# Optimization experiments

Measured on AMD Instinct MI355X. Metric: run time of the kernel, lower is better.

## Reference

```python
import jax, jax.numpy as jnp
import numpy as np

D_MODEL = 1024
NUM_HEADS = 16
HEAD_DIM = D_MODEL // NUM_HEADS


def setup_inputs() -> dict:
    key = jax.random.key(0)
    ks = jax.random.split(key, 9)
    B, S = 4, 2048
    scale = 1.0 / np.sqrt(D_MODEL)
    x = jax.random.normal(ks[0], (B, S, D_MODEL), dtype=jnp.float32)
    Wq = jax.random.normal(ks[1], (D_MODEL, D_MODEL), dtype=jnp.float32) * scale
    bq = jnp.zeros((D_MODEL,), dtype=jnp.float32)
    Wk = jax.random.normal(ks[2], (D_MODEL, D_MODEL), dtype=jnp.float32) * scale
    bk = jnp.zeros((D_MODEL,), dtype=jnp.float32)
    Wv = jax.random.normal(ks[3], (D_MODEL, D_MODEL), dtype=jnp.float32) * scale
    bv = jnp.zeros((D_MODEL,), dtype=jnp.float32)
    Wo = jax.random.normal(ks[4], (D_MODEL, D_MODEL), dtype=jnp.float32) * scale
    bo = jnp.zeros((D_MODEL,), dtype=jnp.float32)
    return {"x": x, "Wq": Wq, "bq": bq, "Wk": Wk, "bk": bk,
            "Wv": Wv, "bv": bv, "Wo": Wo, "bo": bo}


def reference(x, Wq, bq, Wk, bk, Wv, bv, Wo, bo):
    B, S, D = x.shape
    H, Hd = NUM_HEADS, HEAD_DIM
    # linear projections then split heads: [B,S,D] -> [B,H,S,Hd]
    def split(t):
        return t.reshape(B, S, H, Hd).transpose(0, 2, 1, 3)
    q = split(x @ Wq + bq)
    k = split(x @ Wk + bk)
    v = split(x @ Wv + bv)
    scores = jnp.einsum('bhsd,bhtd->bhst', q, k) / jnp.sqrt(
        jnp.asarray(Hd, dtype=jnp.float32))
    attn = jax.nn.softmax(scores, axis=-1)
    out = jnp.einsum('bhst,bhtd->bhsd', attn, v)  # [B,H,S,Hd]
    out = out.transpose(0, 2, 1, 3).reshape(B, S, D)
    return out @ Wo + bo
```

## Files before the change

kernel.cpp:

```cpp
#include <hip/hip_runtime.h>

#define DM 1024
#define NH 16
#define HD 64
#define SEQ 2048
#define BATCH 4
#define MROWS (BATCH*SEQ)

typedef short short8 __attribute__((ext_vector_type(8)));
typedef float f32x4 __attribute__((ext_vector_type(4)));
typedef unsigned short u16x8 __attribute__((ext_vector_type(8)));
typedef unsigned short u16x4 __attribute__((ext_vector_type(4)));

__device__ inline unsigned short f2b(float f) {
    union { float f; unsigned u; } v; v.f = f;
    unsigned r = v.u + 0x7fffu + ((v.u >> 16) & 1u);
    return (unsigned short)(r >> 16);
}

__device__ inline void gload_lds16(const void* g, void* l) {
    __builtin_amdgcn_global_load_lds(
        (const __attribute__((address_space(1))) void*)g,
        (__attribute__((address_space(3))) void*)l, 16, 0, 0);
}

__device__ inline unsigned cvt_pk_bf16(float lo, float hi) {
    unsigned r;
    asm("v_cvt_pk_bf16_f32 %0, %1, %2" : "=v"(r) : "v"(lo), "v"(hi));
    return r;
}

__global__ void k_cvt_x(const float* __restrict__ x, unsigned short* __restrict__ xb) {
    long i = ((long)blockIdx.x * 256 + threadIdx.x) * 8;
    float4 a = *reinterpret_cast<const float4*>(x + i);
    float4 b = *reinterpret_cast<const float4*>(x + i + 4);
    u16x8 o;
    o[0]=f2b(a.x); o[1]=f2b(a.y); o[2]=f2b(a.z); o[3]=f2b(a.w);
    o[4]=f2b(b.x); o[5]=f2b(b.y); o[6]=f2b(b.z); o[7]=f2b(b.w);
    *reinterpret_cast<u16x8*>(xb + i) = o;
}

__global__ void k_cvt_wT(const float* W0, const float* W1, const float* W2, const float* W3,
                         unsigned short* __restrict__ out) {
    const float* Ws[4] = {W0, W1, W2, W3};
    const float* W = Ws[blockIdx.z];
    unsigned short* o = out + (size_t)blockIdx.z * DM * DM;
    __shared__ float t[64][65];
    int tx = threadIdx.x & 15, ty = threadIdx.x >> 4;
    int nb = blockIdx.x * 64, kb = blockIdx.y * 64;
#pragma unroll
    for (int i = 0; i < 4; ++i) {
        int r = ty + 16 * i;
        float4 v = *reinterpret_cast<const float4*>(W + (size_t)(kb + r) * DM + nb + tx * 4);
        t[r][tx*4+0] = v.x; t[r][tx*4+1] = v.y; t[r][tx*4+2] = v.z; t[r][tx*4+3] = v.w;
    }
    __syncthreads();
#pragma unroll
    for (int i = 0; i < 4; ++i) {
        int r = ty + 16 * i;
        u16x4 pv;
#pragma unroll
        for (int j = 0; j < 4; ++j) pv[j] = f2b(t[tx*4+j][r]);
        *reinterpret_cast<u16x4*>(o + (size_t)(nb + r) * DM + kb + tx * 4) = pv;
    }
}

#define BM 128
#define BN 128
#define BK 64
#define QSCALE 0.1803368801f

__global__ __launch_bounds__(256) void k_gemm(const unsigned short* __restrict__ A,
                                              const unsigned short* __restrict__ Bt,
                                              const float* __restrict__ bias,
                                              unsigned short* __restrict__ outb,
                                              float* __restrict__ outf, int mode) {
    __shared__ unsigned short lds[BM*BK + BN*BK];
    unsigned short* lA = lds;
    unsigned short* lB = lds + BM*BK;
    int tid = threadIdx.x, lane = tid & 63, wv = tid >> 6;
    int wr = wv >> 1, wc = wv & 1;
    int c = lane & 15, g = lane >> 4;
    int m0 = blockIdx.x * BM, n0 = blockIdx.y * BN;
    f32x4 acc[4][4] = {};

    for (int kt = 0; kt < DM / BK; ++kt) {
#pragma unroll
        for (int it = 0; it < 4; ++it) {
            int sgi = it * 256 + tid;
            int row = sgi >> 3, blk = sgi & 7;
            int srcoff = kt * BK + ((blk ^ (row & 7)) << 3);
            gload_lds16(A  + (size_t)(m0 + row) * DM + srcoff, &lA[(it*256 + wv*64) * 8]);
            gload_lds16(Bt + (size_t)(n0 + row) * DM + srcoff, &lB[(it*256 + wv*64) * 8]);
        }
        __syncthreads();
#pragma unroll
        for (int ks = 0; ks < 2; ++ks) {
            short8 af[4], bf[4];
#pragma unroll
            for (int mi = 0; mi < 4; ++mi) {
                int row = wr*64 + mi*16 + c;
                af[mi] = *reinterpret_cast<const short8*>(&lA[row*64 + (((ks*4 + g) ^ (row & 7)) << 3)]);
            }
#pragma unroll
            for (int ni = 0; ni < 4; ++ni) {
                int row = wc*64 + ni*16 + c;
                bf[ni] = *reinterpret_cast<const short8*>(&lB[row*64 + (((ks*4 + g) ^ (row & 7)) << 3)]);
            }
#pragma unroll
            for (int mi = 0; mi < 4; ++mi)
#pragma unroll
                for (int ni = 0; ni < 4; ++ni)
                    acc[mi][ni] = __builtin_amdgcn_mfma_f32_16x16x32_bf16(af[mi], bf[ni], acc[mi][ni], 0, 0, 0);
        }
        __syncthreads();
    }

    if (mode == 2) {
        unsigned short* t = lds;
#pragma unroll
        for (int mi = 0; mi < 4; ++mi)
#pragma unroll
            for (int ni = 0; ni < 4; ++ni)
#pragma unroll
                for (int r = 0; r < 4; ++r) {
                    int lr = wr*64 + mi*16 + 4*g + r;
                    int lc = wc*64 + ni*16 + c;
                    t[lc*128 + lr] = f2b(acc[mi][ni][r] + bias[n0 + lc]);
                }
        __syncthreads();
#pragma unroll
        for (int i = 0; i < 8; ++i) {
            int idx = (i*256 + tid) * 8;
            int lc = idx >> 7, lr = idx & 127;
            int gcol = n0 + lc, grow = m0 + lr;
            int b = grow >> 11, s = grow & 2047, h = gcol >> 6, d = gcol & 63;
            *reinterpret_cast<u16x8*>(&outb[((size_t)((b*NH + h) << 6) + d) * SEQ + s]) =
                *reinterpret_cast<u16x8*>(&t[idx]);
        }
    }
}

__global__ __launch_bounds__(512, 2) void k_gemm256(const unsigned short* __restrict__ A,
                                                    const unsigned short* __restrict__ Bt,
                                                    const float* __restrict__ b0,
                                                    const float* __restrict__ b1,
                                                    unsigned short* __restrict__ oQ,
                                                    unsigned short* __restrict__ oK,
                                                    float* __restrict__ oF,
                                                    int perXcd, int mode) {
    __shared__ unsigned short L[2][2][2][128*64];
    int tid = threadIdx.x, lane = tid & 63, wid = tid >> 6;
    int wm = wid >> 2, wn = wid & 3;
    int c = lane & 15, g = lane >> 4;

    int bid = blockIdx.x;
    int swz = (bid & 7) * perXcd + (bid >> 3);
    int mb = swz & 31, nb = swz >> 5;
    int m0 = mb * 256, n0 = nb * 256;

    int idx0 = tid, idx1 = 512 + tid;
    int r0 = idx0 >> 3, k0 = idx0 & 7;
    int r1 = idx1 >> 3, k1 = idx1 & 7;

    auto stageHalf = [&](int buf, int ab, int half, int kt) {
        const unsigned short* src = ab ? Bt : A;
        int base = (ab ? n0 : m0) + half * 128;
        gload_lds16(src + (size_t)(base + r0) * DM + kt*64 + ((k0 ^ (r0 & 7)) << 3),
                    &L[buf][ab][half][idx0 * 8]);
        gload_lds16(src + (size_t)(base + r1) * DM + kt*64 + ((k1 ^ (r1 & 7)) << 3),
                    &L[buf][ab][half][idx1 * 8]);
    };

    f32x4 acc[8][4] = {};
    short8 af[4][2], bf0[2][2], bf1[2][2];

    stageHalf(0, 0, 0, 0); stageHalf(0, 1, 0, 0);
    stageHalf(0, 0, 1, 0); stageHalf(0, 1, 1, 0);

#define RDA(BUF, I, MH, KS) (*reinterpret_cast<const short8*>(                         \
        &L[BUF][0][wm][((MH)*64 + (I)*16 + c)*64 +                                     \
                       ((((KS)*4 + g) ^ (((MH)*64 + (I)*16 + c) & 7)) << 3)]))
#define RDB(BUF, J, NHh, KS) (*reinterpret_cast<const short8*>(                        \
        &L[BUF][1][wn>>1][((wn&1)*64 + (NHh)*32 + (J)*16 + c)*64 +                     \
                       ((((KS)*4 + g) ^ (((wn&1)*64 + (NHh)*32 + (J)*16 + c) & 7)) << 3)]))

    for (int it = 0; it < 16; ++it) {
        int cur = it & 1, nxt = cur ^ 1;

        if (it < 15) {
            stageHalf(nxt, 0, 0, it+1); stageHalf(nxt, 1, 0, it+1);
            stageHalf(nxt, 0, 1, it+1); stageHalf(nxt, 1, 1, it+1);
            asm volatile("s_waitcnt vmcnt(8)" ::: "memory");
        } else {
            asm volatile("s_waitcnt vmcnt(0)" ::: "memory");
        }
        __builtin_amdgcn_s_barrier();

#pragma unroll
        for (int i = 0; i < 4; ++i) { af[i][0] = RDA(cur, i, 0, 0); af[i][1] = RDA(cur, i, 0, 1); }
#pragma unroll
        for (int j = 0; j < 2; ++j) { bf0[j][0] = RDB(cur, j, 0, 0); bf0[j][1] = RDB(cur, j, 0, 1); }
        __builtin_amdgcn_s_setprio(1);
#pragma unroll
        for (int i = 0; i < 4; ++i)
#pragma unroll
            for (int j = 0; j < 2; ++j) {
                acc[i][j] = __builtin_amdgcn_mfma_f32_16x16x32_bf16(af[i][0], bf0[j][0], acc[i][j], 0, 0, 0);
                acc[i][j] = __builtin_amdgcn_mfma_f32_16x16x32_bf16(af[i][1], bf0[j][1], acc[i][j], 0, 0, 0);
            }
        __builtin_amdgcn_s_setprio(0);

#pragma unroll
        for (int i = 0; i < 4; ++i) { af[i][0] = RDA(cur, i, 1, 0); af[i][1] = RDA(cur, i, 1, 1); }
        __builtin_amdgcn_s_setprio(1);
#pragma unroll
        for (int i = 0; i < 4; ++i)
#pragma unroll
            for (int j = 0; j < 2; ++j) {
                acc[4+i][j] = __builtin_amdgcn_mfma_f32_16x16x32_bf16(af[i][0], bf0[j][0], acc[4+i][j], 0, 0, 0);
                acc[4+i][j] = __builtin_amdgcn_mfma_f32_16x16x32_bf16(af[i][1], bf0[j][1], acc[4+i][j], 0, 0, 0);
            }
        __builtin_amdgcn_s_setprio(0);

#pragma unroll
        for (int j = 0; j < 2; ++j) { bf1[j][0] = RDB(cur, j, 1, 0); bf1[j][1] = RDB(cur, j, 1, 1); }
        __builtin_amdgcn_s_setprio(1);
#pragma unroll
        for (int i = 0; i < 4; ++i)
#pragma unroll
            for (int j = 0; j < 2; ++j) {
                acc[4+i][2+j] = __builtin_amdgcn_mfma_f32_16x16x32_bf16(af[i][0], bf1[j][0], acc[4+i][2+j], 0, 0, 0);
                acc[4+i][2+j] = __builtin_amdgcn_mfma_f32_16x16x32_bf16(af[i][1], bf1[j][1], acc[4+i][2+j], 0, 0, 0);
            }
        __builtin_amdgcn_s_setprio(0);

#pragma unroll
        for (int i = 0; i < 4; ++i) { af[i][0] = RDA(cur, i, 0, 0); af[i][1] = RDA(cur, i, 0, 1); }
        __builtin_amdgcn_s_setprio(1);
#pragma unroll
        for (int i = 0; i < 4; ++i)
#pragma unroll
            for (int j = 0; j < 2; ++j) {
                acc[i][2+j] = __builtin_amdgcn_mfma_f32_16x16x32_bf16(af[i][0], bf1[j][0], acc[i][2+j], 0, 0, 0);
                acc[i][2+j] = __builtin_amdgcn_mfma_f32_16x16x32_bf16(af[i][1], bf1[j][1], acc[i][2+j], 0, 0, 0);
            }
        __builtin_amdgcn_s_setprio(0);

        __builtin_amdgcn_s_barrier();
    }
#undef RDA
#undef RDB

    if (mode == 0) {
        int mat = n0 >> 10;
        const float* bias = mat ? b1 : b0;
        unsigned short* outb = mat ? oK : oQ;
        float sc = mat ? 1.0f : QSCALE;
#pragma unroll
        for (int mf = 0; mf < 8; ++mf)
#pragma unroll
            for (int nf = 0; nf < 4; ++nf)
#pragma unroll
                for (int r = 0; r < 4; ++r) {
                    int gr = m0 + wm*128 + mf*16 + 4*g + r;
                    int gc = n0 + wn*64 + nf*16 + c;
                    int gcm = gc & 1023;
                    float v = (acc[mf][nf][r] + bias[gcm]) * sc;
                    int b = gr >> 11, s = gr & 2047, h = gcm >> 6, d = gcm & 63;
                    outb[(((size_t)(b*NH + h) * SEQ + s) << 6) + d] = f2b(v);
                }
    } else {
#pragma unroll
        for (int mf = 0; mf < 8; ++mf)
#pragma unroll
            for (int nf = 0; nf < 4; ++nf)
#pragma unroll
                for (int r = 0; r < 4; ++r) {
                    int gr = m0 + wm*128 + mf*16 + 4*g + r;
                    int gc = n0 + wn*64 + nf*16 + c;
                    oF[(size_t)gr * DM + gc] = acc[mf][nf][r] + b0[gc];
                }
    }
}

__global__ __launch_bounds__(512, 2) void k_gemm_o256(const unsigned short* __restrict__ A,
                                                      const unsigned short* __restrict__ Bt,
                                                      const float* __restrict__ bias,
                                                      float* __restrict__ oF) {
    __shared__ unsigned short L[2][3][128*64];
    int tid = threadIdx.x, lane = tid & 63, wid = tid >> 6;
    int wm = wid >> 2, wn = wid & 3;
    int c = lane & 15, g = lane >> 4;

    int bid = blockIdx.x;
    int swz = (bid & 7) * 32 + (bid >> 3);
    int mb = swz & 31, nb = swz >> 5;
    int m0 = mb * 256, n0 = nb * 128;

    int idx0 = tid, idx1 = 512 + tid;
    int r0 = idx0 >> 3, k0 = idx0 & 7;
    int r1 = idx1 >> 3, k1 = idx1 & 7;

    auto stageA = [&](int buf, int half, int kt) {
        int base = m0 + half * 128;
        gload_lds16(A + (size_t)(base + r0) * DM + kt*64 + ((k0 ^ (r0 & 7)) << 3),
                    &L[buf][half][idx0 * 8]);
        gload_lds16(A + (size_t)(base + r1) * DM + kt*64 + ((k1 ^ (r1 & 7)) << 3),
                    &L[buf][half][idx1 * 8]);
    };
    auto stageB = [&](int buf, int kt) {
        gload_lds16(Bt + (size_t)(n0 + r0) * DM + kt*64 + ((k0 ^ (r0 & 7)) << 3),
                    &L[buf][2][idx0 * 8]);
        gload_lds16(Bt + (size_t)(n0 + r1) * DM + kt*64 + ((k1 ^ (r1 & 7)) << 3),
                    &L[buf][2][idx1 * 8]);
    };

    f32x4 acc[8][2] = {};
    short8 af[4][2], bf[2][2];

    stageA(0, 0, 0); stageA(0, 1, 0); stageB(0, 0);

#define RDA(BUF, I, MH, KS) (*reinterpret_cast<const short8*>(                         \
        &L[BUF][MH][(wm*64 + (I)*16 + c)*64 +                                          \
                    ((((KS)*4 + g) ^ ((wm*64 + (I)*16 + c) & 7)) << 3)]))
#define RDB(BUF, J, KS) (*reinterpret_cast<const short8*>(                             \
        &L[BUF][2][(wn*32 + (J)*16 + c)*64 +                                           \
                   ((((KS)*4 + g) ^ ((wn*32 + (J)*16 + c) & 7)) << 3)]))

    for (int it = 0; it < 16; ++it) {
        int cur = it & 1, nxt = cur ^ 1;

        if (it < 15) {
            stageA(nxt, 0, it+1); stageA(nxt, 1, it+1); stageB(nxt, it+1);
            asm volatile("s_waitcnt vmcnt(6)" ::: "memory");
        } else {
            asm volatile("s_waitcnt vmcnt(0)" ::: "memory");
        }
        __builtin_amdgcn_s_barrier();

#pragma unroll
        for (int i = 0; i < 4; ++i) { af[i][0] = RDA(cur, i, 0, 0); af[i][1] = RDA(cur, i, 0, 1); }
#pragma unroll
        for (int j = 0; j < 2; ++j) { bf[j][0] = RDB(cur, j, 0); bf[j][1] = RDB(cur, j, 1); }
        __builtin_amdgcn_s_setprio(1);
#pragma unroll
        for (int i = 0; i < 4; ++i)
#pragma unroll
            for (int j = 0; j < 2; ++j) {
                acc[i][j] = __builtin_amdgcn_mfma_f32_16x16x32_bf16(af[i][0], bf[j][0], acc[i][j], 0, 0, 0);
                acc[i][j] = __builtin_amdgcn_mfma_f32_16x16x32_bf16(af[i][1], bf[j][1], acc[i][j], 0, 0, 0);
            }
        __builtin_amdgcn_s_setprio(0);

#pragma unroll
        for (int i = 0; i < 4; ++i) { af[i][0] = RDA(cur, i, 1, 0); af[i][1] = RDA(cur, i, 1, 1); }
        __builtin_amdgcn_s_setprio(1);
#pragma unroll
        for (int i = 0; i < 4; ++i)
#pragma unroll
            for (int j = 0; j < 2; ++j) {
                acc[4+i][j] = __builtin_amdgcn_mfma_f32_16x16x32_bf16(af[i][0], bf[j][0], acc[4+i][j], 0, 0, 0);
                acc[4+i][j] = __builtin_amdgcn_mfma_f32_16x16x32_bf16(af[i][1], bf[j][1], acc[4+i][j], 0, 0, 0);
            }
        __builtin_amdgcn_s_setprio(0);

        __builtin_amdgcn_s_barrier();
    }
#undef RDA
#undef RDB

#pragma unroll
    for (int mf = 0; mf < 8; ++mf)
#pragma unroll
        for (int nf = 0; nf < 2; ++nf)
#pragma unroll
            for (int r = 0; r < 4; ++r) {
                int half = mf >> 2, i = mf & 3;
                int gr = m0 + half*128 + wm*64 + i*16 + 4*g + r;
                int gc = n0 + wn*32 + nf*16 + c;
                oF[(size_t)gr * DM + gc] = acc[mf][nf][r] + bias[gc];
            }
}

__global__ __launch_bounds__(256) void k_attn(const unsigned short* __restrict__ Q,
                                              const unsigned short* __restrict__ K,
                                              const unsigned short* __restrict__ VT,
                                              unsigned short* __restrict__ AO) {
    __shared__ unsigned short kt[2][64*64], vt[2][64*64];
    int tid = threadIdx.x, lane = tid & 63, wv = tid >> 6;
    int c = lane & 15, g = lane >> 4;

    int flat = blockIdx.x;
    int nb = (flat & 7) * 256 + (flat >> 3);
    int qb = nb & 31, bh = nb >> 5;

    const unsigned short* Qh = Q  + (size_t)bh * SEQ * HD;
    const unsigned short* Kh = K  + (size_t)bh * SEQ * HD;
    const unsigned short* Vh = VT + (size_t)bh * HD * SEQ;

    int qrow = qb*64 + wv*16 + c;
    short8 qf0 = *reinterpret_cast<const short8*>(&Qh[(size_t)qrow*HD +      g*8]);
    short8 qf1 = *reinterpret_cast<const short8*>(&Qh[(size_t)qrow*HD + 32 + g*8]);

    int row = tid >> 3, blk = tid & 7;
    int xo = (blk ^ (row & 7)) << 3;
    auto srowf = [](int r) {
        return ((r >> 4) & 1)*32 + ((r >> 2) & 3)*8 + ((r >> 5) & 1)*4 + (r & 3);
    };
    const unsigned short* gK0 = Kh + (size_t)srowf(row)      * HD + xo;
    const unsigned short* gK1 = Kh + (size_t)srowf(row + 32) * HD + xo;
    const unsigned short* gV0 = Vh + (size_t)row        * SEQ + xo;
    const unsigned short* gV1 = Vh + (size_t)(row + 32) * SEQ + xo;
    unsigned ldso = wv * 512;

    int swz0 = (g ^ (c & 7)) << 3;
    int swz1 = ((4 + g) ^ (c & 7)) << 3;
    const unsigned short* kb0 = &kt[0][c*64 + swz0];
    const unsigned short* kb1 = &kt[0][c*64 + swz1];
    const unsigned short* vb0 = &vt[0][c*64 + swz0];
    const unsigned short* vb1 = &vt[0][c*64 + swz1];

    float m = -1e30f;
    f32x4 oacc[4] = {}, lacc = {};
    const short ob = (short)0x3F80;
    const short8 ones = {ob, ob, ob, ob, ob, ob, ob, ob};

#define STAGE(SB) do {                                                        \
        gload_lds16(gK0, &kt[SB][ldso]);                                      \
        gload_lds16(gK1, &kt[SB][2048 + ldso]);                               \
        gload_lds16(gV0, &vt[SB][ldso]);                                      \
        gload_lds16(gV1, &vt[SB][2048 + ldso]);                               \
        gK0 += 64*HD; gK1 += 64*HD; gV0 += 64; gV1 += 64;                     \
    } while (0)

#define TILE(BUFO, PRE) do {                                                  \
        PRE;                                                                  \
        f32x4 sacc[4] = {};                                                   \
        __builtin_amdgcn_s_setprio(1);                                        \
        _Pragma("unroll")                                                     \
        for (int nt = 0; nt < 4; ++nt) {                                      \
            short8 kf0 = *reinterpret_cast<const short8*>(kb0 + (BUFO) + nt*1024); \
            short8 kf1 = *reinterpret_cast<const short8*>(kb1 + (BUFO) + nt*1024); \
            sacc[nt] = __builtin_amdgcn_mfma_f32_16x16x32_bf16(kf0, qf0, sacc[nt], 0, 0, 0); \
            sacc[nt] = __builtin_amdgcn_mfma_f32_16x16x32_bf16(kf1, qf1, sacc[nt], 0, 0, 0); \
        }                                                                     \
        __builtin_amdgcn_s_setprio(0);                                        \
        float x0 = fmaxf(fmaxf(sacc[0][0], sacc[0][1]), sacc[0][2]);          \
        float x1 = fmaxf(fmaxf(sacc[0][3], sacc[1][0]), sacc[1][1]);          \
        float x2 = fmaxf(fmaxf(sacc[1][2], sacc[1][3]), sacc[2][0]);          \
        float x3 = fmaxf(fmaxf(sacc[2][1], sacc[2][2]), sacc[2][3]);          \
        float x4 = fmaxf(fmaxf(sacc[3][0], sacc[3][1]), sacc[3][2]);          \
        float tm = fmaxf(fmaxf(fmaxf(x0, x1), fmaxf(x2, x3)), fmaxf(x4, sacc[3][3])); \
        if (__any(tm > m + 8.0f)) {                                           \
            tm = fmaxf(tm, __shfl_xor(tm, 16, 64));                           \
            tm = fmaxf(tm, __shfl_xor(tm, 32, 64));                           \
            float mn = fmaxf(m, tm);                                          \
            float corr = __builtin_amdgcn_exp2f(m - mn);                      \
            m = mn; lacc *= corr;                                             \
            _Pragma("unroll")                                                 \
            for (int ft = 0; ft < 4; ++ft)                                    \
                _Pragma("unroll")                                             \
                for (int r = 0; r < 4; ++r) oacc[ft][r] *= corr;              \
        }                                                                     \
        _Pragma("unroll")                                                     \
        for (int nt = 0; nt < 4; ++nt)                                        \
            _Pragma("unroll")                                                 \
            for (int r = 0; r < 4; ++r)                                       \
                sacc[nt][r] = __builtin_amdgcn_exp2f(sacc[nt][r] - m);        \
        union { unsigned u[4]; short8 v; } U0, U1;                            \
        U0.u[0] = cvt_pk_bf16(sacc[0][0], sacc[0][1]);                        \
        U0.u[1] = cvt_pk_bf16(sacc[0][2], sacc[0][3]);                        \
        U0.u[2] = cvt_pk_bf16(sacc[2][0], sacc[2][1]);                        \
        U0.u[3] = cvt_pk_bf16(sacc[2][2], sacc[2][3]);                        \
        U1.u[0] = cvt_pk_bf16(sacc[1][0], sacc[1][1]);                        \
        U1.u[1] = cvt_pk_bf16(sacc[1][2], sacc[1][3]);                        \
        U1.u[2] = cvt_pk_bf16(sacc[3][0], sacc[3][1]);                        \
        U1.u[3] = cvt_pk_bf16(sacc[3][2], sacc[3][3]);                        \
        short8 pa0 = U0.v, pa1 = U1.v;                                        \
        __builtin_amdgcn_s_setprio(1);                                        \
        _Pragma("unroll")                                                     \
        for (int ft = 0; ft < 4; ++ft) {                                      \
            short8 vf0 = *reinterpret_cast<const short8*>(vb0 + (BUFO) + ft*1024); \
            short8 vf1 = *reinterpret_cast<const short8*>(vb1 + (BUFO) + ft*1024); \
            oacc[ft] = __builtin_amdgcn_mfma_f32_16x16x32_bf16(vf0, pa0, oacc[ft], 0, 0, 0); \
            oacc[ft] = __builtin_amdgcn_mfma_f32_16x16x32_bf16(vf1, pa1, oacc[ft], 0, 0, 0); \
        }                                                                     \
        lacc = __builtin_amdgcn_mfma_f32_16x16x32_bf16(ones, pa0, lacc, 0, 0, 0); \
        lacc = __builtin_amdgcn_mfma_f32_16x16x32_bf16(ones, pa1, lacc, 0, 0, 0); \
        __builtin_amdgcn_s_setprio(0);                                        \
        __syncthreads();                                                      \
    } while (0)

    STAGE(0);
    __syncthreads();

    for (int tp = 0; tp < 15; ++tp) {
        TILE(0,    STAGE(1));
        TILE(4096, STAGE(0));
    }
    TILE(0,    STAGE(1));
    TILE(4096, (void)0);

#undef STAGE
#undef TILE

    int b = bh >> 4, h = bh & 15;
    float inv = 1.f / lacc[0];
#pragma unroll
    for (int ft = 0; ft < 4; ++ft) {
        u16x4 o4;
#pragma unroll
        for (int r = 0; r < 4; ++r) o4[r] = f2b(oacc[ft][r] * inv);
        *reinterpret_cast<u16x4*>(
            &AO[(size_t)(b*SEQ + qrow) * DM + h*HD + ft*16 + 4*g]) = o4;
    }
}

extern "C" void kernel_launch(void* const* d_in, const int* in_sizes, int n_in,
                              void* d_out, int out_size, void* d_ws, size_t ws_size,
                              hipStream_t stream) {
    const float* x  = (const float*)d_in[0];
    const float* Wq = (const float*)d_in[1];
    const float* bq = (const float*)d_in[2];
    const float* Wk = (const float*)d_in[3];
    const float* bk = (const float*)d_in[4];
    const float* Wv = (const float*)d_in[5];
    const float* bv = (const float*)d_in[6];
    const float* Wo = (const float*)d_in[7];
    const float* bo = (const float*)d_in[8];

    char* ws = (char*)d_ws;
    unsigned short* xb  = (unsigned short*)(ws);
    unsigned short* wT  = (unsigned short*)(ws + (16u<<20));
    unsigned short* Qb  = (unsigned short*)(ws + (24u<<20));
    unsigned short* Kb  = (unsigned short*)(ws + (40u<<20));
    unsigned short* VTb = (unsigned short*)(ws + (56u<<20));
    unsigned short* AOb = (unsigned short*)(ws + (72u<<20));

    k_cvt_x<<<dim3(MROWS*DM/8/256), 256, 0, stream>>>(x, xb);
    k_cvt_wT<<<dim3(16,16,4), 256, 0, stream>>>(Wq, Wk, Wv, Wo, wT);

    k_gemm256<<<dim3(256), 512, 0, stream>>>(xb, wT, bq, bk, Qb, Kb, nullptr, 32, 0);

    k_gemm<<<dim3(MROWS/BM, DM/BN), 256, 0, stream>>>(xb, wT + 2*DM*DM, bv, VTb, nullptr, 2);

    k_attn<<<dim3(SEQ/64 * BATCH*NH), 256, 0, stream>>>(Qb, Kb, VTb, AOb);

    k_gemm_o256<<<dim3(256), 512, 0, stream>>>(AOb, wT + 3*DM*DM, bo, (float*)d_out);
}
```

Measured before the change: 199.0 us.

## Load K/V fragments directly from global memory, dropping LDS staging and barriers

```diff
diff --git a/kernel.cpp b/kernel.cpp
--- a/kernel.cpp
+++ b/kernel.cpp
@@ -383,11 +383,10 @@
             }
 }
 
-__global__ __launch_bounds__(256) void k_attn(const unsigned short* __restrict__ Q,
-                                              const unsigned short* __restrict__ K,
-                                              const unsigned short* __restrict__ VT,
-                                              unsigned short* __restrict__ AO) {
-    __shared__ unsigned short kt[2][64*64], vt[2][64*64];
+__global__ __launch_bounds__(256, 4) void k_attn(const unsigned short* __restrict__ Q,
+                                                 const unsigned short* __restrict__ K,
+                                                 const unsigned short* __restrict__ VT,
+                                                 unsigned short* __restrict__ AO) {
     int tid = threadIdx.x, lane = tid & 63, wv = tid >> 6;
     int c = lane & 15, g = lane >> 4;
 
@@ -403,107 +402,99 @@
     short8 qf0 = *reinterpret_cast<const short8*>(&Qh[(size_t)qrow*HD +      g*8]);
     short8 qf1 = *reinterpret_cast<const short8*>(&Qh[(size_t)qrow*HD + 32 + g*8]);
 
-    int row = tid >> 3, blk = tid & 7;
-    int xo = (blk ^ (row & 7)) << 3;
-    auto srowf = [](int r) {
-        return ((r >> 4) & 1)*32 + ((r >> 2) & 3)*8 + ((r >> 5) & 1)*4 + (r & 3);
-    };
-    const unsigned short* gK0 = Kh + (size_t)srowf(row)      * HD + xo;
-    const unsigned short* gK1 = Kh + (size_t)srowf(row + 32) * HD + xo;
-    const unsigned short* gV0 = Vh + (size_t)row        * SEQ + xo;
-    const unsigned short* gV1 = Vh + (size_t)(row + 32) * SEQ + xo;
-    unsigned ldso = wv * 512;
-
-    int swz0 = (g ^ (c & 7)) << 3;
-    int swz1 = ((4 + g) ^ (c & 7)) << 3;
-    const unsigned short* kb0 = &kt[0][c*64 + swz0];
-    const unsigned short* kb1 = &kt[0][c*64 + swz1];
-    const unsigned short* vb0 = &vt[0][c*64 + swz0];
-    const unsigned short* vb1 = &vt[0][c*64 + swz1];
+    int sig = ((c >> 2) << 3) + (c & 3);
+    const unsigned short* pK0 = Kh + (size_t)(sig +  0) * HD + g*8;
+    const unsigned short* pK1 = Kh + (size_t)(sig + 32) * HD + g*8;
+    const unsigned short* pK2 = Kh + (size_t)(sig +  4) * HD + g*8;
+    const unsigned short* pK3 = Kh + (size_t)(sig + 36) * HD + g*8;
+    const unsigned short* pV0 = Vh + (size_t)(c +  0) * SEQ + g*8;
+    const unsigned short* pV1 = Vh + (size_t)(c + 16) * SEQ + g*8;
+    const unsigned short* pV2 = Vh + (size_t)(c + 32) * SEQ + g*8;
+    const unsigned short* pV3 = Vh + (size_t)(c + 48) * SEQ + g*8;
 
     float m = -1e30f;
     f32x4 oacc[4] = {}, lacc = {};
     const short ob = (short)0x3F80;
     const short8 ones = {ob, ob, ob, ob, ob, ob, ob, ob};
 
-#define STAGE(SB) do {                                                        \
-        gload_lds16(gK0, &kt[SB][ldso]);                                      \
-        gload_lds16(gK1, &kt[SB][2048 + ldso]);                               \
-        gload_lds16(gV0, &vt[SB][ldso]);                                      \
-        gload_lds16(gV1, &vt[SB][2048 + ldso]);                               \
-        gK0 += 64*HD; gK1 += 64*HD; gV0 += 64; gV1 += 64;                     \
-    } while (0)
-
-#define TILE(BUFO, PRE) do {                                                  \
-        PRE;                                                                  \
-        f32x4 sacc[4] = {};                                                   \
-        __builtin_amdgcn_s_setprio(1);                                        \
-        _Pragma("unroll")                                                     \
-        for (int nt = 0; nt < 4; ++nt) {                                      \
-            short8 kf0 = *reinterpret_cast<const short8*>(kb0 + (BUFO) + nt*1024); \
-            short8 kf1 = *reinterpret_cast<const short8*>(kb1 + (BUFO) + nt*1024); \
-            sacc[nt] = __builtin_amdgcn_mfma_f32_16x16x32_bf16(kf0, qf0, sacc[nt], 0, 0, 0); \
-            sacc[nt] = __builtin_amdgcn_mfma_f32_16x16x32_bf16(kf1, qf1, sacc[nt], 0, 0, 0); \
-        }                                                                     \
-        __builtin_amdgcn_s_setprio(0);                                        \
-        float x0 = fmaxf(fmaxf(sacc[0][0], sacc[0][1]), sacc[0][2]);          \
-        float x1 = fmaxf(fmaxf(sacc[0][3], sacc[1][0]), sacc[1][1]);          \
-        float x2 = fmaxf(fmaxf(sacc[1][2], sacc[1][3]), sacc[2][0]);          \
-        float x3 = fmaxf(fmaxf(sacc[2][1], sacc[2][2]), sacc[2][3]);          \
-        float x4 = fmaxf(fmaxf(sacc[3][0], sacc[3][1]), sacc[3][2]);          \
-        float tm = fmaxf(fmaxf(fmaxf(x0, x1), fmaxf(x2, x3)), fmaxf(x4, sacc[3][3])); \
-        if (__any(tm > m + 8.0f)) {                                           \
-            tm = fmaxf(tm, __shfl_xor(tm, 16, 64));                           \
-            tm = fmaxf(tm, __shfl_xor(tm, 32, 64));                           \
-            float mn = fmaxf(m, tm);                                          \
-            float corr = __builtin_amdgcn_exp2f(m - mn);                      \
-            m = mn; lacc *= corr;                                             \
-            _Pragma("unroll")                                                 \
-            for (int ft = 0; ft < 4; ++ft)                                    \
-                _Pragma("unroll")                                             \
-                for (int r = 0; r < 4; ++r) oacc[ft][r] *= corr;              \
-        }                                                                     \
-        _Pragma("unroll")                                                     \
-        for (int nt = 0; nt < 4; ++nt)                                        \
-            _Pragma("unroll")                                                 \
-            for (int r = 0; r < 4; ++r)                                       \
-                sacc[nt][r] = __builtin_amdgcn_exp2f(sacc[nt][r] - m);        \
-        union { unsigned u[4]; short8 v; } U0, U1;                            \
-        U0.u[0] = cvt_pk_bf16(sacc[0][0], sacc[0][1]);                        \
-        U0.u[1] = cvt_pk_bf16(sacc[0][2], sacc[0][3]);                        \
-        U0.u[2] = cvt_pk_bf16(sacc[2][0], sacc[2][1]);                        \
-        U0.u[3] = cvt_pk_bf16(sacc[2][2], sacc[2][3]);                        \
-        U1.u[0] = cvt_pk_bf16(sacc[1][0], sacc[1][1]);                        \
-        U1.u[1] = cvt_pk_bf16(sacc[1][2], sacc[1][3]);                        \
-        U1.u[2] = cvt_pk_bf16(sacc[3][0], sacc[3][1]);                        \
-        U1.u[3] = cvt_pk_bf16(sacc[3][2], sacc[3][3]);                        \
-        short8 pa0 = U0.v, pa1 = U1.v;                                        \
-        __builtin_amdgcn_s_setprio(1);                                        \
-        _Pragma("unroll")                                                     \
-        for (int ft = 0; ft < 4; ++ft) {                                      \
-            short8 vf0 = *reinterpret_cast<const short8*>(vb0 + (BUFO) + ft*1024); \
-            short8 vf1 = *reinterpret_cast<const short8*>(vb1 + (BUFO) + ft*1024); \
-            oacc[ft] = __builtin_amdgcn_mfma_f32_16x16x32_bf16(vf0, pa0, oacc[ft], 0, 0, 0); \
-            oacc[ft] = __builtin_amdgcn_mfma_f32_16x16x32_bf16(vf1, pa1, oacc[ft], 0, 0, 0); \
-        }                                                                     \
-        lacc = __builtin_amdgcn_mfma_f32_16x16x32_bf16(ones, pa0, lacc, 0, 0, 0); \
-        lacc = __builtin_amdgcn_mfma_f32_16x16x32_bf16(ones, pa1, lacc, 0, 0, 0); \
-        __builtin_amdgcn_s_setprio(0);                                        \
-        __syncthreads();                                                      \
-    } while (0)
-
-    STAGE(0);
-    __syncthreads();
-
-    for (int tp = 0; tp < 15; ++tp) {
-        TILE(0,    STAGE(1));
-        TILE(4096, STAGE(0));
-    }
-    TILE(0,    STAGE(1));
-    TILE(4096, (void)0);
-
-#undef STAGE
-#undef TILE
+#define RD(P, OFF) (*reinterpret_cast<const short8*>((P) + (OFF)))
+
+    for (int t = 0; t < SEQ/64; ++t) {
+        short8 k00 = RD(pK0, 0), k01 = RD(pK0, 32);
+        short8 k10 = RD(pK1, 0), k11 = RD(pK1, 32);
+        short8 k20 = RD(pK2, 0), k21 = RD(pK2, 32);
+        short8 k30 = RD(pK3, 0), k31 = RD(pK3, 32);
+        f32x4 sacc[4] = {};
+        __builtin_amdgcn_s_setprio(1);
+        sacc[0] = __builtin_amdgcn_mfma_f32_16x16x32_bf16(k00, qf0, sacc[0], 0, 0, 0);
+        sacc[0] = __builtin_amdgcn_mfma_f32_16x16x32_bf16(k01, qf1, sacc[0], 0, 0, 0);
+        sacc[1] = __builtin_amdgcn_mfma_f32_16x16x32_bf16(k10, qf0, sacc[1], 0, 0, 0);
+        sacc[1] = __builtin_amdgcn_mfma_f32_16x16x32_bf16(k11, qf1, sacc[1], 0, 0, 0);
+        sacc[2] = __builtin_amdgcn_mfma_f32_16x16x32_bf16(k20, qf0, sacc[2], 0, 0, 0);
+        sacc[2] = __builtin_amdgcn_mfma_f32_16x16x32_bf16(k21, qf1, sacc[2], 0, 0, 0);
+        sacc[3] = __builtin_amdgcn_mfma_f32_16x16x32_bf16(k30, qf0, sacc[3], 0, 0, 0);
+        sacc[3] = __builtin_amdgcn_mfma_f32_16x16x32_bf16(k31, qf1, sacc[3], 0, 0, 0);
+        __builtin_amdgcn_s_setprio(0);
+
+        short8 v00 = RD(pV0, 0), v01 = RD(pV0, 32);
+        short8 v10 = RD(pV1, 0), v11 = RD(pV1, 32);
+        short8 v20 = RD(pV2, 0), v21 = RD(pV2, 32);
+        short8 v30 = RD(pV3, 0), v31 = RD(pV3, 32);
+
+        float x0 = fmaxf(fmaxf(sacc[0][0], sacc[0][1]), sacc[0][2]);
+        float x1 = fmaxf(fmaxf(sacc[0][3], sacc[1][0]), sacc[1][1]);
+        float x2 = fmaxf(fmaxf(sacc[1][2], sacc[1][3]), sacc[2][0]);
+        float x3 = fmaxf(fmaxf(sacc[2][1], sacc[2][2]), sacc[2][3]);
+        float x4 = fmaxf(fmaxf(sacc[3][0], sacc[3][1]), sacc[3][2]);
+        float tm = fmaxf(fmaxf(fmaxf(x0, x1), fmaxf(x2, x3)), fmaxf(x4, sacc[3][3]));
+
+        if (__any(tm > m + 8.0f)) {
+            tm = fmaxf(tm, __shfl_xor(tm, 16, 64));
+            tm = fmaxf(tm, __shfl_xor(tm, 32, 64));
+            float mn = fmaxf(m, tm);
+            float corr = __builtin_amdgcn_exp2f(m - mn);
+            m = mn;
+            lacc *= corr;
+#pragma unroll
+            for (int ft = 0; ft < 4; ++ft)
+#pragma unroll
+                for (int r = 0; r < 4; ++r) oacc[ft][r] *= corr;
+        }
+
+#pragma unroll
+        for (int nt = 0; nt < 4; ++nt)
+#pragma unroll
+            for (int r = 0; r < 4; ++r)
+                sacc[nt][r] = __builtin_amdgcn_exp2f(sacc[nt][r] - m);
+
+        union { unsigned u[4]; short8 v; } U0, U1;
+        U0.u[0] = cvt_pk_bf16(sacc[0][0], sacc[0][1]);
+        U0.u[1] = cvt_pk_bf16(sacc[0][2], sacc[0][3]);
+        U0.u[2] = cvt_pk_bf16(sacc[2][0], sacc[2][1]);
+        U0.u[3] = cvt_pk_bf16(sacc[2][2], sacc[2][3]);
+        U1.u[0] = cvt_pk_bf16(sacc[1][0], sacc[1][1]);
+        U1.u[1] = cvt_pk_bf16(sacc[1][2], sacc[1][3]);
+        U1.u[2] = cvt_pk_bf16(sacc[3][0], sacc[3][1]);
+        U1.u[3] = cvt_pk_bf16(sacc[3][2], sacc[3][3]);
+        short8 pa0 = U0.v, pa1 = U1.v;
+
+        __builtin_amdgcn_s_setprio(1);
+        oacc[0] = __builtin_amdgcn_mfma_f32_16x16x32_bf16(v00, pa0, oacc[0], 0, 0, 0);
+        oacc[0] = __builtin_amdgcn_mfma_f32_16x16x32_bf16(v01, pa1, oacc[0], 0, 0, 0);
+        oacc[1] = __builtin_amdgcn_mfma_f32_16x16x32_bf16(v10, pa0, oacc[1], 0, 0, 0);
+        oacc[1] = __builtin_amdgcn_mfma_f32_16x16x32_bf16(v11, pa1, oacc[1], 0, 0, 0);
+        oacc[2] = __builtin_amdgcn_mfma_f32_16x16x32_bf16(v20, pa0, oacc[2], 0, 0, 0);
+        oacc[2] = __builtin_amdgcn_mfma_f32_16x16x32_bf16(v21, pa1, oacc[2], 0, 0, 0);
+        oacc[3] = __builtin_amdgcn_mfma_f32_16x16x32_bf16(v30, pa0, oacc[3], 0, 0, 0);
+        oacc[3] = __builtin_amdgcn_mfma_f32_16x16x32_bf16(v31, pa1, oacc[3], 0, 0, 0);
+        lacc = __builtin_amdgcn_mfma_f32_16x16x32_bf16(ones, pa0, lacc, 0, 0, 0);
+        lacc = __builtin_amdgcn_mfma_f32_16x16x32_bf16(ones, pa1, lacc, 0, 0, 0);
+        __builtin_amdgcn_s_setprio(0);
+
+        pK0 += 64*HD; pK1 += 64*HD; pK2 += 64*HD; pK3 += 64*HD;
+        pV0 += 64; pV1 += 64; pV2 += 64; pV3 += 64;
+    }
+#undef RD
 
     int b = bh >> 4, h = bh & 15;
     float inv = 1.f / lacc[0];
```

Result: slower. 551.8 us (+177.3%).
